# Kernel tuning notes

Hardware: AMD Instinct MI355X
Metric: run time of the kernel (lower is better)

The kernel has to match this reference:

```python
import jax, jax.numpy as jnp
import numpy as np

N_HEAD = 16
N_EMBD = 1024
HEAD_DIM = N_EMBD // N_HEAD


def setup_inputs() -> dict:
    key = jax.random.key(0)
    k1, k2, k3 = jax.random.split(key, 3)
    B, T, C = 2, 2048, N_EMBD
    x = jax.random.normal(k1, (B, T, C), dtype=jnp.float32)
    # nn.Linear weights: (out_features, in_features)
    W_attn = jax.random.normal(k2, (3 * C, C), dtype=jnp.float32) * 0.02
    W_proj = jax.random.normal(k3, (C, C), dtype=jnp.float32) * 0.02
    return {"x": x, "W_attn": W_attn, "W_proj": W_proj}


def reference(x, W_attn, W_proj):
    B, T, C = x.shape
    h, hd = N_HEAD, HEAD_DIM
    # c_attn: x @ W^T, then split into q, k, v
    qkv = jnp.einsum('btc,dc->btd', x, W_attn)  # [B, T, 3C]
    q, k, v = jnp.split(qkv, 3, axis=-1)
    # [B, T, C] -> [B, h, T, hd]
    q = q.reshape(B, T, h, hd).transpose(0, 2, 1, 3)
    k = k.reshape(B, T, h, hd).transpose(0, 2, 1, 3)
    v = v.reshape(B, T, h, hd).transpose(0, 2, 1, 3)
    # NOTE: no 1/sqrt(hd) scaling in the original module
    logits = jnp.einsum('bhnk,bhmk->bhnm', q, k)  # [B, h, T, T]
    causal = jnp.tril(jnp.ones((T, T), dtype=bool))  # [T, T]
    logits = jnp.where(causal[None, None, :, :], logits, -jnp.inf)
    weights = jax.nn.softmax(logits, axis=-1)
    O = jnp.einsum('bhnm,bhmv->bhnv', weights, v)  # [B, h, T, hd]
    # Original: einsum('bhnv,hdv->bnd', O, c_proj.weight) with weight viewed as (h, d, v)
    Wp = W_proj.reshape(h, C, hd)
    Y = jnp.einsum('bhnv,hdv->bnd', O, Wp)  # [B, T, C]
    return Y
```

## Files before the change

### kernel.cpp

```cpp
#include <hip/hip_runtime.h>
#include <stdint.h>
#include <math.h>

#define B_    2
#define T_    2048
#define C_    1024
#define H_    16
#define D_    64
#define MTOT  4096
#define NQKV  3072
#define KDIM  1024

#define LOG2E 1.4426950408889634f

typedef short short8 __attribute__((ext_vector_type(8)));
typedef float f32x4  __attribute__((ext_vector_type(4)));

__device__ __forceinline__ uint16_t f2b(float f) {
    union { float f; uint32_t u; } x; x.f = f;
    uint32_t u = x.u;
    return (uint16_t)((u + 0x7FFFu + ((u >> 16) & 1u)) >> 16);
}
__device__ __forceinline__ uint32_t packb2(float a, float b) {
    union { float f; uint32_t u; } x, y; x.f = a; y.f = b;
    return ((x.u + 0x8000u) >> 16) | ((y.u + 0x8000u) & 0xffff0000u);
}
__device__ __forceinline__ uint32_t packb2_rne(float a, float b) {
    return (uint32_t)f2b(a) | ((uint32_t)f2b(b) << 16);
}
__device__ __forceinline__ float fexp2(float x) {
#if __has_builtin(__builtin_amdgcn_exp2f)
    return __builtin_amdgcn_exp2f(x);
#else
    return exp2f(x);
#endif
}

__global__ __launch_bounds__(256) void cast_all(const float* __restrict__ x,
                                                const float* __restrict__ wa,
                                                uint16_t* __restrict__ xb,
                                                uint16_t* __restrict__ wab,
                                                int n4x, int n4w) {
    int i = blockIdx.x * blockDim.x + threadIdx.x;
    const float* src; uint16_t* dst; int j;
    if (i < n4x) { src = x; dst = xb; j = i; }
    else { j = i - n4x; if (j >= n4w) return; src = wa; dst = wab; }
    float4 v = ((const float4*)src)[j];
    ushort4 o;
    o.x = f2b(v.x); o.y = f2b(v.y); o.z = f2b(v.z); o.w = f2b(v.w);
    ((ushort4*)dst)[j] = o;
}

__global__ __launch_bounds__(256) void cast_wp(const float* __restrict__ wp,
                                               uint16_t* __restrict__ wt) {
    int i = blockIdx.x * blockDim.x + threadIdx.x;
    int j4 = (i & 255) * 4;
    int d  = i >> 8;
    int h = j4 >> 6, v = j4 & 63;
    float4 val = *(const float4*)(wp + h * 65536 + d * 64 + v);
    ushort4 o;
    o.x = f2b(val.x); o.y = f2b(val.y); o.z = f2b(val.z); o.w = f2b(val.w);
    *(ushort4*)(wt + d * 1024 + j4) = o;
}

__global__ __launch_bounds__(256, 3) void gemm_qkv(const uint16_t* __restrict__ A,
                                                   const uint16_t* __restrict__ Bw,
                                                   uint16_t* __restrict__ qkvb) {
    __shared__ __align__(16) uint16_t As[128 * 64];
    __shared__ __align__(16) uint16_t Bs[128 * 64];

    int tid = threadIdx.x;
    int w = tid >> 6, lane = tid & 63;
    int qd = lane >> 4, ln = lane & 15;
    int lnx = ln & 7;
    int rowBase = blockIdx.y * 128;
    int colBase = blockIdx.x * 128;
    int mw = (w >> 1) * 64, nw = (w & 1) * 64;

    int srow = tid >> 3;
    int pchunk = tid & 7;
    int gchunk = pchunk ^ (srow & 7);

    const uint16_t* ga = A  + (size_t)(rowBase + srow) * KDIM + gchunk * 8;
    const uint16_t* gb = Bw + (size_t)(colBase + srow) * KDIM + gchunk * 8;
    uint16_t* la = &As[srow * 64 + pchunk * 8];
    uint16_t* lb = &Bs[srow * 64 + pchunk * 8];

    short8 pa[4], pb[4];
#pragma unroll
    for (int m = 0; m < 4; m++) {
        pa[m] = *(const short8*)(ga + (size_t)m * 32 * KDIM);
        pb[m] = *(const short8*)(gb + (size_t)m * 32 * KDIM);
    }

    f32x4 acc[4][4] = {};
    for (int s = 0; s < 16; s++) {
#pragma unroll
        for (int m = 0; m < 4; m++) {
            *(short8*)(la + m * 32 * 64) = pa[m];
            *(short8*)(lb + m * 32 * 64) = pb[m];
        }
        __syncthreads();
        if (s < 15) {
            int k0 = (s + 1) * 64;
#pragma unroll
            for (int m = 0; m < 4; m++) {
                pa[m] = *(const short8*)(ga + k0 + (size_t)m * 32 * KDIM);
                pb[m] = *(const short8*)(gb + k0 + (size_t)m * 32 * KDIM);
            }
        }
#pragma unroll
        for (int ks = 0; ks < 2; ks++) {
            int p = (ks * 4 + qd) ^ lnx;
            short8 a[4], b[4];
#pragma unroll
            for (int i = 0; i < 4; i++) {
                a[i] = *(const short8*)&As[(mw + i * 16 + ln) * 64 + p * 8];
                b[i] = *(const short8*)&Bs[(nw + i * 16 + ln) * 64 + p * 8];
            }
#pragma unroll
            for (int i = 0; i < 4; i++)
#pragma unroll
                for (int j = 0; j < 4; j++)
                    acc[i][j] = __builtin_amdgcn_mfma_f32_16x16x32_bf16(a[i], b[j], acc[i][j], 0, 0, 0);
        }
        __syncthreads();
    }

#pragma unroll
    for (int i = 0; i < 4; i++) {
#pragma unroll
        for (int j = 0; j < 4; j++) {
            int gcol = colBase + nw + j * 16 + ln;
            int which = gcol >> 10;
            int rem = gcol & 1023;
            int h = rem >> 6, d = rem & 63;
            float sc = (which == 0) ? LOG2E : 1.0f;
#pragma unroll
            for (int r = 0; r < 4; r++) {
                int grow = rowBase + mw + i * 16 + qd * 4 + r;
                int bb = grow >> 11, t = grow & 2047;
                uint16_t val = f2b(acc[i][j][r] * sc);
                if (which == 2) {
                    qkvb[(size_t)2 * 4194304 + (((size_t)(bb * H_ + h) * D_) + d) * T_ + t] = val;
                } else {
                    qkvb[(size_t)which * 4194304 + (((size_t)(bb * H_ + h) * T_) + t) * D_ + d] = val;
                }
            }
        }
    }
}


#define STRIP(QS, BQ, OT, LSUM)                                              \
    if (kt * 64 <= (QS) + 15) {                                              \
        bool needm = (kt * 64 + 63 > (QS));                                  \
        f32x4 stt[4];                                                        \
        __builtin_amdgcn_s_setprio(1);                                       \
        _Pragma("unroll")                                                    \
        for (int it = 0; it < 4; it++) {                                     \
            f32x4 z = {};                                                    \
            z = __builtin_amdgcn_mfma_f32_16x16x32_bf16(ak[it][0], (BQ)[0], z, 0, 0, 0); \
            z = __builtin_amdgcn_mfma_f32_16x16x32_bf16(ak[it][1], (BQ)[1], z, 0, 0, 0); \
            stt[it] = z;                                                     \
        }                                                                    \
        __builtin_amdgcn_s_setprio(0);                                       \
        if (needm) {                                                         \
            _Pragma("unroll")                                                \
            for (int it = 0; it < 4; it++)                                   \
                _Pragma("unroll")                                            \
                for (int r = 0; r < 4; r++) {                                \
                    int t = kt * 64 + it * 16 + qd * 4 + r;                  \
                    if (t > (QS) + ln) stt[it][r] = -1.0e30f;                \
                }                                                            \
        }                                                                    \
        _Pragma("unroll")                                                    \
        for (int it = 0; it < 4; it++) {                                     \
            float p0 = fexp2(stt[it][0]);                                    \
            float p1 = fexp2(stt[it][1]);                                    \
            float p2 = fexp2(stt[it][2]);                                    \
            float p3 = fexp2(stt[it][3]);                                    \
            (LSUM) += (p0 + p1) + (p2 + p3);                                 \
            uint2 pk2;                                                       \
            pk2.x = packb2(p0, p1);                                          \
            pk2.y = packb2(p2, p3);                                          \
            *(uint2*)&Pl[w][ln][it * 16 + qd * 4] = pk2;                     \
        }                                                                    \
        short8 bp0 = *(const short8*)&Pl[w][ln][qd * 8];                     \
        short8 bp1 = *(const short8*)&Pl[w][ln][32 + qd * 8];                \
        __builtin_amdgcn_s_setprio(1);                                       \
        _Pragma("unroll")                                                    \
        for (int id = 0; id < 4; id++) {                                     \
            (OT)[id] = __builtin_amdgcn_mfma_f32_16x16x32_bf16(av[id][0], bp0, (OT)[id], 0, 0, 0); \
            (OT)[id] = __builtin_amdgcn_mfma_f32_16x16x32_bf16(av[id][1], bp1, (OT)[id], 0, 0, 0); \
        }                                                                    \
        __builtin_amdgcn_s_setprio(0);                                       \
    }

#define EPI(QS, OT, LSUM)                                                    \
    {                                                                        \
        float ssum = (LSUM);                                                 \
        ssum += __shfl_xor(ssum, 16);                                        \
        ssum += __shfl_xor(ssum, 32);                                        \
        float rl = 1.0f / ssum;                                              \
        int q = (QS) + ln;                                                   \
        _Pragma("unroll")                                                    \
        for (int id = 0; id < 4; id++) {                                     \
            float v0 = (OT)[id][0] * rl;                                     \
            float v1 = (OT)[id][1] * rl;                                     \
            float v2 = (OT)[id][2] * rl;                                     \
            float v3 = (OT)[id][3] * rl;                                     \
            uint2 pk2;                                                       \
            pk2.x = packb2_rne(v0, v1);                                      \
            pk2.y = packb2_rne(v2, v3);                                      \
            *(uint2*)&oc[(size_t)(b * T_ + q) * C_ + h * 64 + id * 16 + qd * 4] = pk2; \
        }                                                                    \
    }

__global__ __launch_bounds__(512, 2) void attn(const uint16_t* __restrict__ qkvb,
                                               uint16_t* __restrict__ oc) {
    __shared__ __align__(16) uint16_t Ks[2][64 * 64];
    __shared__ __align__(16) uint16_t Vs[2][64 * 64];
    __shared__ __align__(16) uint16_t Pl[8][16][72];

    int tid = threadIdx.x;
    int w = tid >> 6, lane = tid & 63;
    int qd = lane >> 4, ln = lane & 15;
    int lnx = ln & 7;
    int bid = blockIdx.x;
    int j = bid >> 5;
    int bh = bid & 31;
    int b = bh >> 4, h = bh & 15;

    const uint16_t* Q0 = qkvb + (size_t)bh * T_ * D_;
    const uint16_t* K  = Q0 + 4194304;
    const uint16_t* Vt = qkvb + (size_t)2 * 4194304 + (size_t)bh * D_ * T_;

    int qsA = j * 128 + w * 16;
    int qsB = (15 - j) * 128 + w * 16;
    int nt  = 32 - 2 * j;

    short8 bqA[2], bqB[2];
#pragma unroll
    for (int ks = 0; ks < 2; ks++) {
        bqA[ks] = *(const short8*)(Q0 + (size_t)(qsA + ln) * D_ + ks * 32 + qd * 8);
        bqB[ks] = *(const short8*)(Q0 + (size_t)(qsB + ln) * D_ + ks * 32 + qd * 8);
    }

    int srow = tid >> 3;
    int pch = tid & 7;
    int gch = pch ^ (srow & 7);
    const uint16_t* gk = K  + (size_t)srow * D_ + gch * 8;
    const uint16_t* gv = Vt + (size_t)srow * T_ + gch * 8;
    int lofs = srow * 64 + pch * 8;

    short8 pk = *(const short8*)gk;
    short8 pv = *(const short8*)gv;

    f32x4 otA[4] = {}, otB[4] = {};
    float lA = 0.f, lB = 0.f;

    int c = 0;
    for (int kt = 0; kt < nt; kt++) {
        *(short8*)&Ks[c][lofs] = pk;
        *(short8*)&Vs[c][lofs] = pv;
        __syncthreads();
        if (kt + 1 < nt) {
            pk = *(const short8*)(gk + (size_t)(kt + 1) * 64 * D_);
            pv = *(const short8*)(gv + (size_t)(kt + 1) * 64);
        }
        short8 ak[4][2], av[4][2];
#pragma unroll
        for (int ks = 0; ks < 2; ks++) {
            int p8 = ((ks * 4 + qd) ^ lnx) * 8;
#pragma unroll
            for (int it = 0; it < 4; it++) {
                ak[it][ks] = *(const short8*)&Ks[c][(it * 16 + ln) * 64 + p8];
                av[it][ks] = *(const short8*)&Vs[c][(it * 16 + ln) * 64 + p8];
            }
        }
        STRIP(qsA, bqA, otA, lA);
        STRIP(qsB, bqB, otB, lB);
        c ^= 1;
    }

    EPI(qsA, otA, lA);
    EPI(qsB, otB, lB);
}

__global__ __launch_bounds__(256, 3) void gemm_out(const uint16_t* __restrict__ A,
                                                   const uint16_t* __restrict__ Bw,
                                                   float* __restrict__ out) {
    __shared__ __align__(16) uint16_t As[128 * 64];
    __shared__ __align__(16) uint16_t Bs[64 * 64];

    int tid = threadIdx.x;
    int w = tid >> 6, lane = tid & 63;
    int qd = lane >> 4, ln = lane & 15;
    int lnx = ln & 7;
    int rowBase = blockIdx.y * 128;
    int colBase = blockIdx.x * 64;
    int mw = (w >> 1) * 64, nw = (w & 1) * 32;

    int srow = tid >> 3;
    int pchunk = tid & 7;
    int gchunk = pchunk ^ (srow & 7);

    const uint16_t* ga = A  + (size_t)(rowBase + srow) * KDIM + gchunk * 8;
    const uint16_t* gb = Bw + (size_t)(colBase + srow) * KDIM + gchunk * 8;
    uint16_t* la = &As[srow * 64 + pchunk * 8];
    uint16_t* lb = &Bs[srow * 64 + pchunk * 8];

    short8 pa[4], pb[2];
#pragma unroll
    for (int m = 0; m < 4; m++)
        pa[m] = *(const short8*)(ga + (size_t)m * 32 * KDIM);
#pragma unroll
    for (int m = 0; m < 2; m++)
        pb[m] = *(const short8*)(gb + (size_t)m * 32 * KDIM);

    f32x4 acc[4][2] = {};
    for (int s = 0; s < 16; s++) {
#pragma unroll
        for (int m = 0; m < 4; m++)
            *(short8*)(la + m * 32 * 64) = pa[m];
#pragma unroll
        for (int m = 0; m < 2; m++)
            *(short8*)(lb + m * 32 * 64) = pb[m];
        __syncthreads();
        if (s < 15) {
            int k0 = (s + 1) * 64;
#pragma unroll
            for (int m = 0; m < 4; m++)
                pa[m] = *(const short8*)(ga + k0 + (size_t)m * 32 * KDIM);
#pragma unroll
            for (int m = 0; m < 2; m++)
                pb[m] = *(const short8*)(gb + k0 + (size_t)m * 32 * KDIM);
        }
#pragma unroll
        for (int ks = 0; ks < 2; ks++) {
            int p = (ks * 4 + qd) ^ lnx;
            short8 a[4], b[2];
#pragma unroll
            for (int i = 0; i < 4; i++)
                a[i] = *(const short8*)&As[(mw + i * 16 + ln) * 64 + p * 8];
#pragma unroll
            for (int j = 0; j < 2; j++)
                b[j] = *(const short8*)&Bs[(nw + j * 16 + ln) * 64 + p * 8];
#pragma unroll
            for (int i = 0; i < 4; i++)
#pragma unroll
                for (int j = 0; j < 2; j++)
                    acc[i][j] = __builtin_amdgcn_mfma_f32_16x16x32_bf16(a[i], b[j], acc[i][j], 0, 0, 0);
        }
        __syncthreads();
    }

#pragma unroll
    for (int i = 0; i < 4; i++)
#pragma unroll
        for (int j = 0; j < 2; j++)
#pragma unroll
            for (int r = 0; r < 4; r++) {
                int grow = rowBase + mw + i * 16 + qd * 4 + r;
                int gcol = colBase + nw + j * 16 + ln;
                out[(size_t)grow * 1024 + gcol] = acc[i][j][r];
            }
}

extern "C" void kernel_launch(void* const* d_in, const int* in_sizes, int n_in,
                              void* d_out, int out_size, void* d_ws, size_t ws_size,
                              hipStream_t stream) {
    const float* x  = (const float*)d_in[0];
    const float* Wa = (const float*)d_in[1];
    const float* Wp = (const float*)d_in[2];
    float* out = (float*)d_out;

    uint16_t* ws   = (uint16_t*)d_ws;
    uint16_t* xb   = ws;
    uint16_t* Wab  = xb + 4194304;
    uint16_t* Wtb  = Wab + 3145728;
    uint16_t* qkvb = Wtb + 1048576;
    uint16_t* ob   = qkvb + (size_t)3 * 4194304;

    cast_all<<<7168, 256, 0, stream>>>(x, Wa, xb, Wab, 4194304 / 4, 3145728 / 4);
    cast_wp<<<1024, 256, 0, stream>>>(Wp, Wtb);
    gemm_qkv<<<dim3(24, 32), 256, 0, stream>>>(xb, Wab, qkvb);
    attn<<<256, 512, 0, stream>>>(qkvb, ob);
    gemm_out<<<dim3(16, 32), 256, 0, stream>>>(ob, Wtb, out);
}
```

Measured before the change: 168.0 us.

## Restructure QKV GEMM into 256x256 tiles with double-buffered direct-to-LDS loads

The QKV projection GEMM now uses 512-thread blocks with 256x256 output tiles. Operands are staged with global_load_lds straight into double-buffered LDS, replacing the register round-trip. Explicit vmcnt waits and barriers let the next K-slice load overlap the current MFMA work, and s_setprio raises priority around the MFMA bursts. The larger tile improves data reuse, but the grid drops to 192 blocks, fewer than the CU count, and LDS use per block rises to 128 KB, which limits occupancy.

```diff
diff --git a/kernel.cpp b/kernel.cpp
--- a/kernel.cpp
+++ b/kernel.cpp
@@ -34,6 +34,12 @@
 #else
     return exp2f(x);
 #endif
+}
+
+__device__ __forceinline__ void gload16(const uint16_t* g, uint16_t* l) {
+    __builtin_amdgcn_global_load_lds((const __attribute__((address_space(1))) uint32_t*)g,
+                                     (__attribute__((address_space(3))) uint32_t*)l,
+                                     16, 0, 0);
 }
 
 __global__ __launch_bounds__(256) void cast_all(const float* __restrict__ x,
@@ -63,82 +69,105 @@
     *(ushort4*)(wt + d * 1024 + j4) = o;
 }
 
-__global__ __launch_bounds__(256, 3) void gemm_qkv(const uint16_t* __restrict__ A,
+__global__ __launch_bounds__(512, 2) void gemm_qkv(const uint16_t* __restrict__ A,
                                                    const uint16_t* __restrict__ Bw,
                                                    uint16_t* __restrict__ qkvb) {
-    __shared__ __align__(16) uint16_t As[128 * 64];
-    __shared__ __align__(16) uint16_t Bs[128 * 64];
+    __shared__ __align__(16) uint16_t As[2][256 * 64];
+    __shared__ __align__(16) uint16_t Bs[2][256 * 64];
 
     int tid = threadIdx.x;
     int w = tid >> 6, lane = tid & 63;
     int qd = lane >> 4, ln = lane & 15;
     int lnx = ln & 7;
-    int rowBase = blockIdx.y * 128;
-    int colBase = blockIdx.x * 128;
-    int mw = (w >> 1) * 64, nw = (w & 1) * 64;
-
-    int srow = tid >> 3;
-    int pchunk = tid & 7;
-    int gchunk = pchunk ^ (srow & 7);
-
-    const uint16_t* ga = A  + (size_t)(rowBase + srow) * KDIM + gchunk * 8;
-    const uint16_t* gb = Bw + (size_t)(colBase + srow) * KDIM + gchunk * 8;
-    uint16_t* la = &As[srow * 64 + pchunk * 8];
-    uint16_t* lb = &Bs[srow * 64 + pchunk * 8];
-
-    short8 pa[4], pb[4];
-#pragma unroll
-    for (int m = 0; m < 4; m++) {
-        pa[m] = *(const short8*)(ga + (size_t)m * 32 * KDIM);
-        pb[m] = *(const short8*)(gb + (size_t)m * 32 * KDIM);
-    }
-
-    f32x4 acc[4][4] = {};
+    int wm = w >> 2, wn = w & 3;
+    int rowBase = blockIdx.y * 256;
+    int colBase = blockIdx.x * 256;
+
+    int l8 = lane >> 3, l7 = lane & 7;
+    int gch = l7 ^ l8;
+    const uint16_t* ga = A  + (size_t)(rowBase + w * 8 + l8) * KDIM + gch * 8;
+    const uint16_t* gb = Bw + (size_t)(colBase + w * 8 + l8) * KDIM + gch * 8;
+    int lofs = (w * 8) * 64;
+
+#define STG(buf, kk)                                                             \
+    {   int k0_ = (kk) * 64;                                                     \
+        _Pragma("unroll")                                                        \
+        for (int m = 0; m < 4; m++)                                              \
+            gload16(ga + k0_ + (size_t)m * 64 * KDIM, &As[buf][lofs + m * 64 * 64]); \
+        _Pragma("unroll")                                                        \
+        for (int m = 0; m < 4; m++)                                              \
+            gload16(gb + k0_ + (size_t)m * 64 * KDIM, &Bs[buf][lofs + m * 64 * 64]); }
+
+    f32x4 acc[8][4] = {};
+    STG(0, 0);
+    STG(1, 1);
+    asm volatile("s_waitcnt vmcnt(8)" ::: "memory");
+    __builtin_amdgcn_s_barrier();
+    asm volatile("" ::: "memory");
+
     for (int s = 0; s < 16; s++) {
-#pragma unroll
-        for (int m = 0; m < 4; m++) {
-            *(short8*)(la + m * 32 * 64) = pa[m];
-            *(short8*)(lb + m * 32 * 64) = pb[m];
-        }
-        __syncthreads();
-        if (s < 15) {
-            int k0 = (s + 1) * 64;
-#pragma unroll
-            for (int m = 0; m < 4; m++) {
-                pa[m] = *(const short8*)(ga + k0 + (size_t)m * 32 * KDIM);
-                pb[m] = *(const short8*)(gb + k0 + (size_t)m * 32 * KDIM);
+        int cur = s & 1;
+        const uint16_t* Ab = &As[cur][0];
+        const uint16_t* Bb = &Bs[cur][0];
+
+        short8 b[4][2];
+#pragma unroll
+        for (int j = 0; j < 4; j++)
+#pragma unroll
+            for (int ks = 0; ks < 2; ks++) {
+                int p = (ks * 4 + qd) ^ lnx;
+                b[j][ks] = *(const short8*)&Bb[(wn * 64 + j * 16 + ln) * 64 + p * 8];
             }
-        }
-#pragma unroll
-        for (int ks = 0; ks < 2; ks++) {
-            int p = (ks * 4 + qd) ^ lnx;
-            short8 a[4], b[4];
-#pragma unroll
-            for (int i = 0; i < 4; i++) {
-                a[i] = *(const short8*)&As[(mw + i * 16 + ln) * 64 + p * 8];
-                b[i] = *(const short8*)&Bs[(nw + i * 16 + ln) * 64 + p * 8];
-            }
-#pragma unroll
-            for (int i = 0; i < 4; i++)
-#pragma unroll
-                for (int j = 0; j < 4; j++)
-                    acc[i][j] = __builtin_amdgcn_mfma_f32_16x16x32_bf16(a[i], b[j], acc[i][j], 0, 0, 0);
-        }
-        __syncthreads();
-    }
-
-#pragma unroll
-    for (int i = 0; i < 4; i++) {
+#pragma unroll
+        for (int q = 0; q < 4; q++) {
+            short8 a[2][2];
+#pragma unroll
+            for (int im = 0; im < 2; im++)
+#pragma unroll
+                for (int ks = 0; ks < 2; ks++) {
+                    int p = (ks * 4 + qd) ^ lnx;
+                    a[im][ks] = *(const short8*)&Ab[(wm * 128 + (q * 2 + im) * 16 + ln) * 64 + p * 8];
+                }
+            __builtin_amdgcn_s_setprio(1);
+#pragma unroll
+            for (int ks = 0; ks < 2; ks++)
+#pragma unroll
+                for (int im = 0; im < 2; im++)
+#pragma unroll
+                    for (int j = 0; j < 4; j++)
+                        acc[q * 2 + im][j] = __builtin_amdgcn_mfma_f32_16x16x32_bf16(
+                            a[im][ks], b[j][ks], acc[q * 2 + im][j], 0, 0, 0);
+            __builtin_amdgcn_s_setprio(0);
+        }
+
+        asm volatile("" ::: "memory");
+        __builtin_amdgcn_s_barrier();
+        asm volatile("" ::: "memory");
+        if (s + 2 < 16) {
+            STG(cur, s + 2);
+            asm volatile("s_waitcnt vmcnt(8)" ::: "memory");
+        } else if (s + 1 < 16) {
+            asm volatile("s_waitcnt vmcnt(0)" ::: "memory");
+        }
+        if (s + 1 < 16) {
+            __builtin_amdgcn_s_barrier();
+            asm volatile("" ::: "memory");
+        }
+    }
+#undef STG
+
+    int which = colBase >> 10;
+    float sc = (which == 0) ? LOG2E : 1.0f;
+#pragma unroll
+    for (int i = 0; i < 8; i++) {
 #pragma unroll
         for (int j = 0; j < 4; j++) {
-            int gcol = colBase + nw + j * 16 + ln;
-            int which = gcol >> 10;
+            int gcol = colBase + wn * 64 + j * 16 + ln;
             int rem = gcol & 1023;
             int h = rem >> 6, d = rem & 63;
-            float sc = (which == 0) ? LOG2E : 1.0f;
 #pragma unroll
             for (int r = 0; r < 4; r++) {
-                int grow = rowBase + mw + i * 16 + qd * 4 + r;
+                int grow = rowBase + wm * 128 + i * 16 + qd * 4 + r;
                 int bb = grow >> 11, t = grow & 2047;
                 uint16_t val = f2b(acc[i][j][r] * sc);
                 if (which == 2) {
@@ -385,7 +414,7 @@
 
     cast_all<<<7168, 256, 0, stream>>>(x, Wa, xb, Wab, 4194304 / 4, 3145728 / 4);
     cast_wp<<<1024, 256, 0, stream>>>(Wp, Wtb);
-    gemm_qkv<<<dim3(24, 32), 256, 0, stream>>>(xb, Wab, qkvb);
+    gemm_qkv<<<dim3(12, 16), 512, 0, stream>>>(xb, Wab, qkvb);
     attn<<<256, 512, 0, stream>>>(qkvb, ob);
     gemm_out<<<dim3(16, 32), 256, 0, stream>>>(ob, Wtb, out);
 }
```

Result: slower. 191.9 us (+14.2%).

## Fuse fp32-to-bf16 casts into GEMM tile loads and drop cast kernels

Applied to the files above, without the earlier changes.

Removes the separate cast_all and cast_wp kernels. The QKV GEMM now loads fp32 x and W_attn directly and converts them to bf16 while staging into shared memory. The output GEMM reads W_proj in fp32 with the head-transposed indexing folded into its load addresses. This saves two launches and a bf16 round trip through global memory, but the GEMMs now read twice as many bytes per tile, repeated across blocks, and hold more registers for prefetch.

```diff
diff --git a/kernel.cpp b/kernel.cpp
--- a/kernel.cpp
+++ b/kernel.cpp
@@ -28,6 +28,14 @@
 __device__ __forceinline__ uint32_t packb2_rne(float a, float b) {
     return (uint32_t)f2b(a) | ((uint32_t)f2b(b) << 16);
 }
+__device__ __forceinline__ short8 cvt8(float4 a, float4 b) {
+    union { short8 s; uint32_t u[4]; } r;
+    r.u[0] = packb2_rne(a.x, a.y);
+    r.u[1] = packb2_rne(a.z, a.w);
+    r.u[2] = packb2_rne(b.x, b.y);
+    r.u[3] = packb2_rne(b.z, b.w);
+    return r.s;
+}
 __device__ __forceinline__ float fexp2(float x) {
 #if __has_builtin(__builtin_amdgcn_exp2f)
     return __builtin_amdgcn_exp2f(x);
@@ -36,35 +44,8 @@
 #endif
 }
 
-__global__ __launch_bounds__(256) void cast_all(const float* __restrict__ x,
-                                                const float* __restrict__ wa,
-                                                uint16_t* __restrict__ xb,
-                                                uint16_t* __restrict__ wab,
-                                                int n4x, int n4w) {
-    int i = blockIdx.x * blockDim.x + threadIdx.x;
-    const float* src; uint16_t* dst; int j;
-    if (i < n4x) { src = x; dst = xb; j = i; }
-    else { j = i - n4x; if (j >= n4w) return; src = wa; dst = wab; }
-    float4 v = ((const float4*)src)[j];
-    ushort4 o;
-    o.x = f2b(v.x); o.y = f2b(v.y); o.z = f2b(v.z); o.w = f2b(v.w);
-    ((ushort4*)dst)[j] = o;
-}
-
-__global__ __launch_bounds__(256) void cast_wp(const float* __restrict__ wp,
-                                               uint16_t* __restrict__ wt) {
-    int i = blockIdx.x * blockDim.x + threadIdx.x;
-    int j4 = (i & 255) * 4;
-    int d  = i >> 8;
-    int h = j4 >> 6, v = j4 & 63;
-    float4 val = *(const float4*)(wp + h * 65536 + d * 64 + v);
-    ushort4 o;
-    o.x = f2b(val.x); o.y = f2b(val.y); o.z = f2b(val.z); o.w = f2b(val.w);
-    *(ushort4*)(wt + d * 1024 + j4) = o;
-}
-
-__global__ __launch_bounds__(256, 3) void gemm_qkv(const uint16_t* __restrict__ A,
-                                                   const uint16_t* __restrict__ Bw,
+__global__ __launch_bounds__(256, 3) void gemm_qkv(const float* __restrict__ A,
+                                                   const float* __restrict__ Bw,
                                                    uint16_t* __restrict__ qkvb) {
     __shared__ __align__(16) uint16_t As[128 * 64];
     __shared__ __align__(16) uint16_t Bs[128 * 64];
@@ -81,32 +62,36 @@
     int pchunk = tid & 7;
     int gchunk = pchunk ^ (srow & 7);
 
-    const uint16_t* ga = A  + (size_t)(rowBase + srow) * KDIM + gchunk * 8;
-    const uint16_t* gb = Bw + (size_t)(colBase + srow) * KDIM + gchunk * 8;
+    const float* ga = A  + (size_t)(rowBase + srow) * KDIM + gchunk * 8;
+    const float* gb = Bw + (size_t)(colBase + srow) * KDIM + gchunk * 8;
     uint16_t* la = &As[srow * 64 + pchunk * 8];
     uint16_t* lb = &Bs[srow * 64 + pchunk * 8];
 
-    short8 pa[4], pb[4];
+    float4 pa[4][2], pb[4][2];
 #pragma unroll
     for (int m = 0; m < 4; m++) {
-        pa[m] = *(const short8*)(ga + (size_t)m * 32 * KDIM);
-        pb[m] = *(const short8*)(gb + (size_t)m * 32 * KDIM);
+        pa[m][0] = *(const float4*)(ga + (size_t)m * 32 * KDIM);
+        pa[m][1] = *(const float4*)(ga + (size_t)m * 32 * KDIM + 4);
+        pb[m][0] = *(const float4*)(gb + (size_t)m * 32 * KDIM);
+        pb[m][1] = *(const float4*)(gb + (size_t)m * 32 * KDIM + 4);
     }
 
     f32x4 acc[4][4] = {};
     for (int s = 0; s < 16; s++) {
 #pragma unroll
         for (int m = 0; m < 4; m++) {
-            *(short8*)(la + m * 32 * 64) = pa[m];
-            *(short8*)(lb + m * 32 * 64) = pb[m];
+            *(short8*)(la + m * 32 * 64) = cvt8(pa[m][0], pa[m][1]);
+            *(short8*)(lb + m * 32 * 64) = cvt8(pb[m][0], pb[m][1]);
         }
         __syncthreads();
         if (s < 15) {
             int k0 = (s + 1) * 64;
 #pragma unroll
             for (int m = 0; m < 4; m++) {
-                pa[m] = *(const short8*)(ga + k0 + (size_t)m * 32 * KDIM);
-                pb[m] = *(const short8*)(gb + k0 + (size_t)m * 32 * KDIM);
+                pa[m][0] = *(const float4*)(ga + k0 + (size_t)m * 32 * KDIM);
+                pa[m][1] = *(const float4*)(ga + k0 + (size_t)m * 32 * KDIM + 4);
+                pb[m][0] = *(const float4*)(gb + k0 + (size_t)m * 32 * KDIM);
+                pb[m][1] = *(const float4*)(gb + k0 + (size_t)m * 32 * KDIM + 4);
             }
         }
 #pragma unroll
@@ -289,7 +274,7 @@
 }
 
 __global__ __launch_bounds__(256, 3) void gemm_out(const uint16_t* __restrict__ A,
-                                                   const uint16_t* __restrict__ Bw,
+                                                   const float* __restrict__ Wp,
                                                    float* __restrict__ out) {
     __shared__ __align__(16) uint16_t As[128 * 64];
     __shared__ __align__(16) uint16_t Bs[64 * 64];
@@ -306,18 +291,23 @@
     int pchunk = tid & 7;
     int gchunk = pchunk ^ (srow & 7);
 
-    const uint16_t* ga = A  + (size_t)(rowBase + srow) * KDIM + gchunk * 8;
-    const uint16_t* gb = Bw + (size_t)(colBase + srow) * KDIM + gchunk * 8;
+    const uint16_t* ga = A + (size_t)(rowBase + srow) * KDIM + gchunk * 8;
+    int j0 = gchunk * 8;
+    int hh = j0 >> 6, vv = j0 & 63;
+    const float* gbf = Wp + (size_t)hh * 65536 + (size_t)(colBase + srow) * 64 + vv;
     uint16_t* la = &As[srow * 64 + pchunk * 8];
     uint16_t* lb = &Bs[srow * 64 + pchunk * 8];
 
-    short8 pa[4], pb[2];
+    short8 pa[4];
+    float4 pbf[2][2];
 #pragma unroll
     for (int m = 0; m < 4; m++)
         pa[m] = *(const short8*)(ga + (size_t)m * 32 * KDIM);
 #pragma unroll
-    for (int m = 0; m < 2; m++)
-        pb[m] = *(const short8*)(gb + (size_t)m * 32 * KDIM);
+    for (int m = 0; m < 2; m++) {
+        pbf[m][0] = *(const float4*)(gbf + (size_t)m * 32 * 64);
+        pbf[m][1] = *(const float4*)(gbf + (size_t)m * 32 * 64 + 4);
+    }
 
     f32x4 acc[4][2] = {};
     for (int s = 0; s < 16; s++) {
@@ -326,7 +316,7 @@
             *(short8*)(la + m * 32 * 64) = pa[m];
 #pragma unroll
         for (int m = 0; m < 2; m++)
-            *(short8*)(lb + m * 32 * 64) = pb[m];
+            *(short8*)(lb + m * 32 * 64) = cvt8(pbf[m][0], pbf[m][1]);
         __syncthreads();
         if (s < 15) {
             int k0 = (s + 1) * 64;
@@ -334,8 +324,10 @@
             for (int m = 0; m < 4; m++)
                 pa[m] = *(const short8*)(ga + k0 + (size_t)m * 32 * KDIM);
 #pragma unroll
-            for (int m = 0; m < 2; m++)
-                pb[m] = *(const short8*)(gb + k0 + (size_t)m * 32 * KDIM);
+            for (int m = 0; m < 2; m++) {
+                pbf[m][0] = *(const float4*)(gbf + (size_t)(s + 1) * 65536 + (size_t)m * 32 * 64);
+                pbf[m][1] = *(const float4*)(gbf + (size_t)(s + 1) * 65536 + (size_t)m * 32 * 64 + 4);
+            }
         }
 #pragma unroll
         for (int ks = 0; ks < 2; ks++) {
@@ -377,15 +369,10 @@
     float* out = (float*)d_out;
 
     uint16_t* ws   = (uint16_t*)d_ws;
-    uint16_t* xb   = ws;
-    uint16_t* Wab  = xb + 4194304;
-    uint16_t* Wtb  = Wab + 3145728;
-    uint16_t* qkvb = Wtb + 1048576;
+    uint16_t* qkvb = ws;
     uint16_t* ob   = qkvb + (size_t)3 * 4194304;
 
-    cast_all<<<7168, 256, 0, stream>>>(x, Wa, xb, Wab, 4194304 / 4, 3145728 / 4);
-    cast_wp<<<1024, 256, 0, stream>>>(Wp, Wtb);
-    gemm_qkv<<<dim3(24, 32), 256, 0, stream>>>(xb, Wab, qkvb);
+    gemm_qkv<<<dim3(24, 32), 256, 0, stream>>>(x, Wa, qkvb);
     attn<<<256, 512, 0, stream>>>(qkvb, ob);
-    gemm_out<<<dim3(16, 32), 256, 0, stream>>>(ob, Wtb, out);
-}
+    gemm_out<<<dim3(16, 32), 256, 0, stream>>>(ob, Wp, out);
+}
```

Measured after the change: 178.5 us. 1.06x slower.
